# Optimization experiments

Hardware: AMD Instinct MI355X
Metric: run time of the kernel (lower is better)

The kernel has to match this reference:

```python
import jax, jax.numpy as jnp
import numpy as np

N, E, F, DH, R = 50000, 800000, 128, 128, 6  # nodes, edges, in-feat, hidden, relations (heads=1)
EPS = 1e-5
NEG_SLOPE = 0.01


def setup_inputs() -> dict:
    key = jax.random.key(0)
    ks = jax.random.split(key, 20)
    sF = 1.0 / np.sqrt(F)
    sD = 1.0 / np.sqrt(DH)
    return {
        "x": jax.random.normal(ks[0], (N, F), dtype=jnp.float32),
        "edge_index": jax.random.randint(ks[1], (2, E), 0, N, dtype=jnp.int64),
        "edge_type": jax.random.randint(ks[2], (E,), 0, R, dtype=jnp.int64),
        # RGCNConv params
        "rgcn_w": jax.random.normal(ks[3], (R, F, DH), dtype=jnp.float32) * sF,
        "rgcn_root": jax.random.normal(ks[4], (F, DH), dtype=jnp.float32) * sF,
        "rgcn_bias": jnp.zeros((DH,), dtype=jnp.float32),
        # TransformerConv params (heads=1, concat=True)
        "wq": jax.random.normal(ks[5], (DH, DH), dtype=jnp.float32) * sD,
        "bq": jnp.zeros((DH,), dtype=jnp.float32),
        "wk": jax.random.normal(ks[6], (DH, DH), dtype=jnp.float32) * sD,
        "bk": jnp.zeros((DH,), dtype=jnp.float32),
        "wv": jax.random.normal(ks[7], (DH, DH), dtype=jnp.float32) * sD,
        "bv": jnp.zeros((DH,), dtype=jnp.float32),
        "wskip": jax.random.normal(ks[8], (DH, DH), dtype=jnp.float32) * sD,
        "bskip": jnp.zeros((DH,), dtype=jnp.float32),
        # BatchNorm1d params (training-mode batch stats)
        "bn_gamma": jnp.ones((DH,), dtype=jnp.float32),
        "bn_beta": jnp.zeros((DH,), dtype=jnp.float32),
    }


def _rgcn(x, src, dst, edge_type, w, root, bias):
    # PyG RGCNConv: per-relation mean aggregation of x_j @ W_r over incoming edges, + root + bias
    out = x @ root + bias  # [N, DH]
    for r in range(R):
        m = (edge_type == r)
        xw = x @ w[r]  # [N, DH]
        msg = jnp.where(m[:, None], xw[src], 0.0)  # [E, DH]
        s = jax.ops.segment_sum(msg, dst, num_segments=N)
        cnt = jax.ops.segment_sum(m.astype(x.dtype), dst, num_segments=N)
        out = out + s / jnp.maximum(cnt, 1.0)[:, None]
    return out


def _transformer_conv(x, src, dst, wq, bq, wk, bk, wv, bv, wskip, bskip):
    # PyG TransformerConv, heads=1: edge-softmax attention over incoming edges + skip projection
    q = x @ wq + bq  # [N, DH]
    k = x @ wk + bk
    v = x @ wv + bv
    score = jnp.sum(q[dst] * k[src], axis=-1) / jnp.sqrt(jnp.asarray(DH, x.dtype))  # [E]
    smax = jax.ops.segment_max(score, dst, num_segments=N)  # -inf for empty segments (unused)
    a = jnp.exp(score - smax[dst])
    denom = jax.ops.segment_sum(a, dst, num_segments=N)
    alpha = a / denom[dst]  # every edge's dst has >=1 edge, denom > 0
    agg = jax.ops.segment_sum(alpha[:, None] * v[src], dst, num_segments=N)  # [N, DH]
    return agg + (x @ wskip + bskip)


def reference(x, edge_index, edge_type, rgcn_w, rgcn_root, rgcn_bias,
              wq, bq, wk, bk, wv, bv, wskip, bskip, bn_gamma, bn_beta):
    src, dst = edge_index[0], edge_index[1]
    h = _rgcn(x, src, dst, edge_type, rgcn_w, rgcn_root, rgcn_bias)
    h = _transformer_conv(h, src, dst, wq, bq, wk, bk, wv, bv, wskip, bskip)
    # BatchNorm1d (training: batch statistics, biased variance)
    mu = jnp.mean(h, axis=0)
    var = jnp.mean(jnp.square(h - mu), axis=0)
    h = bn_gamma * (h - mu) * jax.lax.rsqrt(var + EPS) + bn_beta
    return jnp.where(h > 0, h, NEG_SLOPE * h)
```

## Files before the change

### kernel.cpp

```cpp
#include <hip/hip_runtime.h>
#include <hip/hip_bf16.h>
#include <math.h>

#define FDIM 128
#define NREL 6

typedef _Float16 half8 __attribute__((ext_vector_type(8)));
typedef _Float16 h16x2 __attribute__((ext_vector_type(2)));
typedef float f32x4 __attribute__((ext_vector_type(4)));

#if __has_builtin(__builtin_amdgcn_fdot2)
#define FDOT2(A, B, C) __builtin_amdgcn_fdot2((A), (B), (C), false)
#else
#define FDOT2(A, B, C) ((float)(A)[0] * (float)(B)[0] + ((float)(A)[1] * (float)(B)[1] + (C)))
#endif

static __device__ __forceinline__ unsigned short f2h(float f) {
  union { _Float16 h; unsigned short u; } p; p.h = (_Float16)f; return p.u;
}

__global__ void cvt_x_kernel(const float* __restrict__ x, unsigned short* __restrict__ xh,
                             int n4) {
  int i = blockIdx.x * 256 + threadIdx.x;
  if (i < n4) {
    float4 v = ((const float4*)x)[i];
    union { _Float16 h[4]; uint2 u; } p;
    p.h[0] = (_Float16)v.x; p.h[1] = (_Float16)v.y;
    p.h[2] = (_Float16)v.z; p.h[3] = (_Float16)v.w;
    ((uint2*)xh)[i] = p.u;
  }
}

__global__ void cvt_wr_kernel(const float* __restrict__ root, const float* __restrict__ w,
                              unsigned short* __restrict__ bt) {
  int i = blockIdx.x * 256 + threadIdx.x;
  if (i < 896 * 128) {
    int n = i / 896, kk = i - n * 896;
    float v = (kk < 128) ? root[kk * 128 + n] : w[(long long)(kk - 128) * 128 + n];
    bt[i] = f2h(v);
  }
}

struct WPtrs { const float* W[4]; };
__global__ void cvt_wq_kernel(WPtrs wp, unsigned short* __restrict__ bt) {
  int i = blockIdx.x * 256 + threadIdx.x;
  if (i < 4 * 128 * 128) {
    int z = i >> 14;
    int r = i & 16383;
    int n = r >> 7, kk = r & 127;
    bt[i] = f2h(wp.W[z][kk * 128 + n]);
  }
}

struct GArgs {
  const unsigned short* Ax;
  const unsigned short* Aagg;
  const unsigned short* BtR;
  const unsigned short* BtQ;
  const float* biasR;
  const float* bias2[4];
  unsigned short* qh; unsigned short* kh; unsigned short* vh; float* sk;
  int M;
};

__launch_bounds__(256)
__global__ void gemm_fused(GArgs g) {
  __shared__ unsigned short Ah[64 * 64];
  __shared__ unsigned short Bh[128 * 64];
  __shared__ unsigned short hL[64 * 128];
  const int tid = threadIdx.x;
  const int lane = tid & 63;
  const int wid = tid >> 6;
  const int wm = wid >> 1, wn = wid & 1;
  const int lr = lane & 15, lk = lane >> 4;
  const int m0 = blockIdx.x * 64;
  const int M = g.M;

  f32x4 acc[2][4];
#pragma unroll
  for (int a = 0; a < 2; ++a)
#pragma unroll
    for (int b = 0; b < 4; ++b) { acc[a][b][0] = 0.f; acc[a][b][1] = 0.f; acc[a][b][2] = 0.f; acc[a][b][3] = 0.f; }

  for (int k0 = 0; k0 < 896; k0 += 64) {
    __syncthreads();
#pragma unroll
    for (int p = 0; p < 2; ++p) {
      int idx = tid + 256 * p;
      int r = idx >> 3, c = idx & 7;
      int row = m0 + r; if (row > M - 1) row = M - 1;
      const unsigned short* srcp =
          (k0 < 128) ? (g.Ax + (long long)row * 128 + k0 + c * 8)
                     : (g.Aagg + (long long)row * 768 + (k0 - 128) + c * 8);
      uint4 u = *(const uint4*)srcp;
      ((uint4*)Ah)[r * 8 + (c ^ (r & 7))] = u;
    }
#pragma unroll
    for (int p = 0; p < 4; ++p) {
      int idx = tid + 256 * p;
      int rn = idx >> 3, c = idx & 7;
      uint4 u = *(const uint4*)(g.BtR + (long long)rn * 896 + k0 + c * 8);
      ((uint4*)Bh)[rn * 8 + (c ^ (rn & 7))] = u;
    }
    __syncthreads();
#pragma unroll
    for (int ks = 0; ks < 2; ++ks) {
      half8 a[2], b[4];
#pragma unroll
      for (int fm = 0; fm < 2; ++fm) {
        int row = wm * 32 + fm * 16 + lr;
        a[fm] = *(const half8*)&((uint4*)Ah)[row * 8 + ((ks * 4 + lk) ^ (row & 7))];
      }
#pragma unroll
      for (int fn = 0; fn < 4; ++fn) {
        int col = wn * 64 + fn * 16 + lr;
        b[fn] = *(const half8*)&((uint4*)Bh)[col * 8 + ((ks * 4 + lk) ^ (col & 7))];
      }
#pragma unroll
      for (int fm = 0; fm < 2; ++fm)
#pragma unroll
        for (int fn = 0; fn < 4; ++fn)
          acc[fm][fn] = __builtin_amdgcn_mfma_f32_16x16x32_f16(a[fm], b[fn], acc[fm][fn], 0, 0, 0);
    }
  }

#pragma unroll
  for (int fm = 0; fm < 2; ++fm) {
#pragma unroll
    for (int fn = 0; fn < 4; ++fn) {
      int col = wn * 64 + fn * 16 + lr;
      float bv = g.biasR[col];
      int cu = col >> 3, cb = col & 7;
#pragma unroll
      for (int j = 0; j < 4; ++j) {
        int row = wm * 32 + fm * 16 + lk * 4 + j;
        float vv = acc[fm][fn][j] + bv;
        hL[row * 128 + ((cu ^ (row & 7)) << 3) + cb] = f2h(vv);
      }
    }
  }

  const float CF = 0.08838834764831845f * 1.4426950408889634f;
  const float* b2 = (wid == 0) ? g.bias2[0]
                  : (wid == 1) ? g.bias2[1]
                  : (wid == 2) ? g.bias2[2] : g.bias2[3];
#pragma unroll
  for (int half = 0; half < 2; ++half) {
    f32x4 acc2[4][4];
#pragma unroll
    for (int a = 0; a < 4; ++a)
#pragma unroll
      for (int b = 0; b < 4; ++b) { acc2[a][b][0] = 0.f; acc2[a][b][1] = 0.f; acc2[a][b][2] = 0.f; acc2[a][b][3] = 0.f; }

#pragma unroll
    for (int ks = 0; ks < 4; ++ks) {
      __syncthreads();
#pragma unroll
      for (int p = 0; p < 4; ++p) {
        int u = tid + 256 * p;
        int zz = u >> 8, n = (u >> 2) & 63, c = u & 3;
        uint4 w = *(const uint4*)(g.BtQ + (long long)zz * 16384 +
                                  (long long)(half * 64 + n) * 128 + ks * 32 + c * 8);
        ((uint4*)Bh)[zz * 256 + n * 4 + (c ^ (n & 3))] = w;
      }
      __syncthreads();
      half8 a[4], b[4];
#pragma unroll
      for (int fm = 0; fm < 4; ++fm) {
        int row = fm * 16 + lr;
        a[fm] = *(const half8*)&((uint4*)hL)[row * 16 + ((ks * 4 + lk) ^ (row & 7))];
      }
#pragma unroll
      for (int fn = 0; fn < 4; ++fn) {
        int n = fn * 16 + lr;
        b[fn] = *(const half8*)&((uint4*)Bh)[wid * 256 + n * 4 + (lk ^ (n & 3))];
      }
#pragma unroll
      for (int fm = 0; fm < 4; ++fm)
#pragma unroll
        for (int fn = 0; fn < 4; ++fn)
          acc2[fm][fn] = __builtin_amdgcn_mfma_f32_16x16x32_f16(a[fm], b[fn], acc2[fm][fn], 0, 0, 0);
    }

#pragma unroll
    for (int fm = 0; fm < 4; ++fm) {
#pragma unroll
      for (int fn = 0; fn < 4; ++fn) {
        int col = half * 64 + fn * 16 + lr;
        float bv = b2[col];
#pragma unroll
        for (int j = 0; j < 4; ++j) {
          int row = m0 + fm * 16 + lk * 4 + j;
          if (row < M) {
            float vv = acc2[fm][fn][j] + bv;
            long long off = (long long)row * 128 + col;
            if (wid == 0) g.qh[off] = f2h(vv * CF);
            else if (wid == 1) g.kh[off] = f2h(vv);
            else if (wid == 2) g.vh[off] = f2h(vv);
            else g.sk[off] = vv;
          }
        }
      }
    }
  }
}

__global__ void hist_kernel(const int* __restrict__ dst, const int* __restrict__ etype,
                            int* __restrict__ cnt, int E) {
  int e = blockIdx.x * blockDim.x + threadIdx.x;
  if (e < E) atomicAdd(&cnt[dst[e] * NREL + etype[e]], 1);
}

__launch_bounds__(1024)
__global__ void scan1(const int* __restrict__ deg, int* __restrict__ incl,
                      int* __restrict__ part, int n) {
  __shared__ int sh[1024];
  int tid = threadIdx.x;
  int i = blockIdx.x * 1024 + tid;
  sh[tid] = (i < n) ? deg[i] : 0;
  __syncthreads();
  for (int o = 1; o < 1024; o <<= 1) {
    int t = (tid >= o) ? sh[tid - o] : 0;
    __syncthreads();
    sh[tid] += t;
    __syncthreads();
  }
  if (i < n) incl[i] = sh[tid];
  if (tid == 1023) part[blockIdx.x] = sh[1023];
}

__global__ void scan2(int* part, int nb) {
  int lane = threadIdx.x;
  int run = 0;
  for (int b0 = 0; b0 < nb; b0 += 64) {
    int i = b0 + lane;
    int orig = (i < nb) ? part[i] : 0;
    int v = orig;
#pragma unroll
    for (int o = 1; o < 64; o <<= 1) {
      int t = __shfl_up(v, o);
      if (lane >= o) v += t;
    }
    if (i < nb) part[i] = run + v - orig;
    run += __shfl(v, 63);
  }
}

__global__ void scan3(const int* __restrict__ incl, const int* __restrict__ part,
                      int* __restrict__ offs, int n) {
  int i = blockIdx.x * blockDim.x + threadIdx.x;
  if (i < n) {
    offs[i + 1] = incl[i] + part[i >> 10];
    if (i == 0) offs[0] = 0;
  }
}

__global__ void scatter_kernel(const int* __restrict__ src, const int* __restrict__ dst,
                               const int* __restrict__ etype, const int* __restrict__ offs6,
                               int* __restrict__ cur, int* __restrict__ csrc, int E) {
  int e = blockIdx.x * blockDim.x + threadIdx.x;
  if (e < E) {
    int key = dst[e] * NREL + etype[e];
    int p = offs6[key] + atomicAdd(&cur[key], 1);
    csrc[p] = src[e] << 8;
  }
}

__launch_bounds__(256)
__global__ void rgcn_agg(const unsigned short* __restrict__ xh, const int* __restrict__ offs6,
                         const int* __restrict__ csrc,
                         unsigned short* __restrict__ aggh, int N) {
  int node = blockIdx.x * 4 + (threadIdx.x >> 6);
  if (node >= N) return;
  int lane = threadIdx.x & 63;
  const char* xc = (const char*)xh;
  const int* bp = offs6 + node * NREL;
  const int b0 = bp[0];
  int bn0 = bp[1], bn1 = bp[2], bn2 = bp[3], bn3 = bp[4], bn4 = bp[5], bn5 = bp[6];
  const int b6 = bn5;
  unsigned* ap = (unsigned*)(aggh + (long long)node * (NREL * FDIM)) + lane;

  float tx = 0.f, ty = 0.f;
  float px = 0.f, py = 0.f;
  int bprev = b0, snaps = 0;

#define FLUSH(EPOS)                                                          \
  while (snaps < NREL && bn0 == (EPOS)) {                                    \
    int cnt_ = (EPOS) - bprev;                                               \
    float inv_ = cnt_ ? 1.f / (float)cnt_ : 0.f;                             \
    union { _Float16 h[2]; unsigned u; } pk_;                                \
    pk_.h[0] = (_Float16)((tx - px) * inv_);                                 \
    pk_.h[1] = (_Float16)((ty - py) * inv_);                                 \
    *ap = pk_.u; ap += 64;                                                   \
    px = tx; py = ty; bprev = (EPOS); ++snaps;                               \
    bn0 = bn1; bn1 = bn2; bn2 = bn3; bn3 = bn4; bn4 = bn5;                   \
  }

#define EAT(XU)                                                              \
  {                                                                          \
    union { unsigned u; _Float16 h[2]; } c_; c_.u = (XU);                    \
    tx += (float)c_.h[0]; ty += (float)c_.h[1];                              \
  }

  FLUSH(b0)
  int e = b0;
  for (; e + 16 <= b6; e += 16) {
    unsigned xv[16];
#pragma unroll
    for (int t = 0; t < 16; ++t)
      xv[t] = ((const unsigned*)(xc + csrc[e + t]))[lane];
    EAT(xv[0])  FLUSH(e + 1)   EAT(xv[1])  FLUSH(e + 2)
    EAT(xv[2])  FLUSH(e + 3)   EAT(xv[3])  FLUSH(e + 4)
    EAT(xv[4])  FLUSH(e + 5)   EAT(xv[5])  FLUSH(e + 6)
    EAT(xv[6])  FLUSH(e + 7)   EAT(xv[7])  FLUSH(e + 8)
    EAT(xv[8])  FLUSH(e + 9)   EAT(xv[9])  FLUSH(e + 10)
    EAT(xv[10]) FLUSH(e + 11)  EAT(xv[11]) FLUSH(e + 12)
    EAT(xv[12]) FLUSH(e + 13)  EAT(xv[13]) FLUSH(e + 14)
    EAT(xv[14]) FLUSH(e + 15)  EAT(xv[15]) FLUSH(e + 16)
  }
  for (; e + 4 <= b6; e += 4) {
    unsigned y0 = ((const unsigned*)(xc + csrc[e + 0]))[lane];
    unsigned y1 = ((const unsigned*)(xc + csrc[e + 1]))[lane];
    unsigned y2 = ((const unsigned*)(xc + csrc[e + 2]))[lane];
    unsigned y3 = ((const unsigned*)(xc + csrc[e + 3]))[lane];
    EAT(y0) FLUSH(e + 1) EAT(y1) FLUSH(e + 2)
    EAT(y2) FLUSH(e + 3) EAT(y3) FLUSH(e + 4)
  }
  for (; e < b6; ++e) {
    unsigned xv = ((const unsigned*)(xc + csrc[e]))[lane];
    EAT(xv) FLUSH(e + 1)
  }
#undef EAT
#undef FLUSH
}

__launch_bounds__(256)
__global__ void attn_kernel(const unsigned short* __restrict__ qh,
                            const unsigned short* __restrict__ kh,
                            const unsigned short* __restrict__ vh,
                            const int* __restrict__ offs6, const int* __restrict__ csrc,
                            float* __restrict__ out,
                            float* __restrict__ gsumB, float* __restrict__ gsqB, int N) {
  __shared__ float bsum[4][FDIM];
  __shared__ float bsq[4][FDIM];
  int wv = threadIdx.x >> 6;
  int node = blockIdx.x * 4 + wv;
  int lane = threadIdx.x & 63;
  bool active = (node < N);
  int start = 0, end = 0;
  if (active) { start = offs6[node * NREL]; end = offs6[node * NREL + NREL]; }
  int deg = end - start;

  const int g16 = lane >> 4;
  const int f = lane & 15;
  const char* kc = (const char*)kh;
  const char* vc = (const char*)vh;

  union U4 { uint4 u; h16x2 h[4]; };
  U4 qf;
  if (active) qf.u = *(const uint4*)(qh + (long long)node * FDIM + f * 8);

  float m = -INFINITY, den = 0.f, acc0 = 0.f, acc1 = 0.f;

#define LOADQ(E0, S0, S1, S2, S3, KU, V0, V1, V2, V3)                        \
  {                                                                          \
    S0 = csrc[(E0) + (g16 ^ 0)];                                             \
    S1 = csrc[(E0) + (g16 ^ 1)];                                             \
    S2 = csrc[(E0) + (g16 ^ 2)];                                             \
    S3 = csrc[(E0) + (g16 ^ 3)];                                             \
    KU = *(const uint4*)(kc + S0 + f * 16);                                  \
    V0 = ((const unsigned*)(vc + S0))[lane];                                 \
    V1 = ((const unsigned*)(vc + S1))[lane];                                 \
    V2 = ((const unsigned*)(vc + S2))[lane];                                 \
    V3 = ((const unsigned*)(vc + S3))[lane];                                 \
  }

#define PROCESS(KU, V0, V1, V2, V3, MASKED, M0, M1, M2, M3)                  \
  {                                                                          \
    U4 kf; kf.u = KU;                                                        \
    float pd = FDOT2(qf.h[0], kf.h[0], 0.f);                                 \
    pd = FDOT2(qf.h[1], kf.h[1], pd);                                        \
    pd = FDOT2(qf.h[2], kf.h[2], pd);                                        \
    pd = FDOT2(qf.h[3], kf.h[3], pd);                                        \
    pd += __shfl_xor(pd, 1);  pd += __shfl_xor(pd, 2);                       \
    pd += __shfl_xor(pd, 4);  pd += __shfl_xor(pd, 8);                       \
    float sc0 = pd;                                                          \
    float sc1 = __shfl_xor(pd, 16);                                          \
    float sc2 = __shfl_xor(pd, 32);                                          \
    float sc3 = __shfl_xor(pd, 48);                                          \
    if (MASKED) {                                                            \
      if (!(M0)) sc0 = -INFINITY;                                            \
      if (!(M1)) sc1 = -INFINITY;                                            \
      if (!(M2)) sc2 = -INFINITY;                                            \
      if (!(M3)) sc3 = -INFINITY;                                            \
    }                                                                        \
    float mx = fmaxf(fmaxf(sc0, sc1), fmaxf(sc2, sc3));                      \
    float mn = fmaxf(m, mx);                                                 \
    float scl = exp2f(m - mn);                                               \
    float a0 = exp2f(sc0 - mn), a1 = exp2f(sc1 - mn);                        \
    float a2 = exp2f(sc2 - mn), a3 = exp2f(sc3 - mn);                        \
    den = den * scl + ((a0 + a1) + (a2 + a3));                               \
    union { unsigned u; _Float16 h[2]; } w0, w1, w2, w3;                     \
    w0.u = V0; w1.u = V1; w2.u = V2; w3.u = V3;                              \
    acc0 = acc0 * scl + a0 * (float)w0.h[0] + a1 * (float)w1.h[0]            \
                      + a2 * (float)w2.h[0] + a3 * (float)w3.h[0];           \
    acc1 = acc1 * scl + a0 * (float)w0.h[1] + a1 * (float)w1.h[1]            \
                      + a2 * (float)w2.h[1] + a3 * (float)w3.h[1];           \
    m = mn;                                                                  \
  }

  if (deg > 0) {
    int nfull4 = deg & ~3;
    int e = start;
    if (nfull4 > 0) {
      int sA0, sA1, sA2, sA3; uint4 kA; unsigned vA0, vA1, vA2, vA3;
      LOADQ(e, sA0, sA1, sA2, sA3, kA, vA0, vA1, vA2, vA3)
      for (; e < start + nfull4; e += 4) {
        int sB0, sB1, sB2, sB3; uint4 kB; unsigned vB0, vB1, vB2, vB3;
        bool more = (e + 4 < start + nfull4);
        if (more) LOADQ(e + 4, sB0, sB1, sB2, sB3, kB, vB0, vB1, vB2, vB3)
        PROCESS(kA, vA0, vA1, vA2, vA3, false, 1, 1, 1, 1)
        if (more) { kA = kB; vA0 = vB0; vA1 = vB1; vA2 = vB2; vA3 = vB3; }
      }
    }
    int rem = deg & 3;
    if (rem) {
      int e0 = start + nfull4;
      int j0 = g16 ^ 0, j1 = g16 ^ 1, j2 = g16 ^ 2, j3 = g16 ^ 3;
      int sT0 = csrc[e0 + (j0 < rem ? j0 : 0)];
      int sT1 = csrc[e0 + (j1 < rem ? j1 : 0)];
      int sT2 = csrc[e0 + (j2 < rem ? j2 : 0)];
      int sT3 = csrc[e0 + (j3 < rem ? j3 : 0)];
      uint4 kT = *(const uint4*)(kc + sT0 + f * 16);
      unsigned vT0 = ((const unsigned*)(vc + sT0))[lane];
      unsigned vT1 = ((const unsigned*)(vc + sT1))[lane];
      unsigned vT2 = ((const unsigned*)(vc + sT2))[lane];
      unsigned vT3 = ((const unsigned*)(vc + sT3))[lane];
      PROCESS(kT, vT0, vT1, vT2, vT3, true, j0 < rem, j1 < rem, j2 < rem, j3 < rem)
    }
  }
#undef LOADQ
#undef PROCESS

  float2 o = make_float2(0.f, 0.f);
  if (active) {
    float2* op = (float2*)(out + (long long)node * FDIM);
    o = op[lane];
    if (deg > 0) {
      float inv = 1.f / den;
      o.x += acc0 * inv;
      o.y += acc1 * inv;
      op[lane] = o;
    }
  }

  ((float2*)bsum[wv])[lane] = make_float2(o.x, o.y);
  ((float2*)bsq[wv])[lane]  = make_float2(o.x * o.x, o.y * o.y);
  __syncthreads();
  if (threadIdx.x < FDIM) {
    int d = threadIdx.x;
    float s  = bsum[0][d] + bsum[1][d] + bsum[2][d] + bsum[3][d];
    float q2 = bsq[0][d]  + bsq[1][d]  + bsq[2][d]  + bsq[3][d];
    int bucket = blockIdx.x & 31;
    atomicAdd(&gsumB[bucket * FDIM + d], s);
    atomicAdd(&gsqB[bucket * FDIM + d], q2);
  }
}

__global__ void bn_final(const float* __restrict__ gsumB, const float* __restrict__ gsqB,
                         const float* __restrict__ gamma, const float* __restrict__ beta,
                         float* __restrict__ ss, int N) {
  int d = threadIdx.x;
  if (d < FDIM) {
    float s = 0.f, q = 0.f;
    for (int b = 0; b < 32; ++b) { s += gsumB[b * FDIM + d]; q += gsqB[b * FDIM + d]; }
    float mean = s / (float)N;
    float var = q / (float)N - mean * mean;
    var = fmaxf(var, 0.f);
    float sc = gamma[d] * rsqrtf(var + 1e-5f);
    ss[d] = sc;
    ss[FDIM + d] = beta[d] - mean * sc;
  }
}

__global__ void bn_apply(float* __restrict__ x, const float* __restrict__ ss, long long total4) {
  long long i = (long long)blockIdx.x * blockDim.x + threadIdx.x;
  if (i < total4) {
    int d0 = (int)((i * 4) & (FDIM - 1));
    float4 vv = ((const float4*)x)[i];
    float y0 = ss[d0 + 0] * vv.x + ss[FDIM + d0 + 0];
    float y1 = ss[d0 + 1] * vv.y + ss[FDIM + d0 + 1];
    float y2 = ss[d0 + 2] * vv.z + ss[FDIM + d0 + 2];
    float y3 = ss[d0 + 3] * vv.w + ss[FDIM + d0 + 3];
    vv.x = (y0 > 0.f) ? y0 : 0.01f * y0;
    vv.y = (y1 > 0.f) ? y1 : 0.01f * y1;
    vv.z = (y2 > 0.f) ? y2 : 0.01f * y2;
    vv.w = (y3 > 0.f) ? y3 : 0.01f * y3;
    ((float4*)x)[i] = vv;
  }
}

extern "C" void kernel_launch(void* const* d_in, const int* in_sizes, int n_in,
                              void* d_out, int out_size, void* d_ws, size_t ws_size,
                              hipStream_t stream) {
  const float* x         = (const float*)d_in[0];
  const int*   ei        = (const int*)d_in[1];
  const int*   etype     = (const int*)d_in[2];
  const float* rgcn_w    = (const float*)d_in[3];
  const float* rgcn_root = (const float*)d_in[4];
  const float* rgcn_bias = (const float*)d_in[5];
  const float* wq = (const float*)d_in[6];  const float* bq = (const float*)d_in[7];
  const float* wk = (const float*)d_in[8];  const float* bk = (const float*)d_in[9];
  const float* wv = (const float*)d_in[10]; const float* bv = (const float*)d_in[11];
  const float* wsk = (const float*)d_in[12]; const float* bsk = (const float*)d_in[13];
  const float* gamma = (const float*)d_in[14]; const float* beta = (const float*)d_in[15];

  const int N = in_sizes[0] / FDIM;
  const int E = in_sizes[1] / 2;
  const int* src = ei;
  const int* dst = ei + E;
  const int NK = N * NREL;

  char* base = (char*)d_ws;
  size_t off = 0;
  auto alloc = [&](size_t bytes) -> char* {
    char* p = base + off;
    off += (bytes + 255) & ~(size_t)255;
    return p;
  };
  unsigned short* aggh = (unsigned short*)alloc((size_t)N * (NREL * FDIM) * 2);
  unsigned short* qbuf = aggh;
  unsigned short* kbuf = aggh + (size_t)N * FDIM;
  unsigned short* vbuf = aggh + 2 * (size_t)N * FDIM;
  unsigned short* xh   = (unsigned short*)alloc((size_t)N * FDIM * 2);
  unsigned short* btR  = (unsigned short*)alloc((size_t)896 * 128 * 2);
  unsigned short* btQ  = (unsigned short*)alloc((size_t)4 * 128 * 128 * 2);
  int* cnt6 = (int*)alloc((size_t)2 * NK * 4);
  int* cur  = cnt6 + NK;
  int* offs6 = (int*)alloc((size_t)(NK + 1) * 4);
  int* incl = (int*)alloc((size_t)NK * 4);
  int* part = (int*)alloc((size_t)512 * 4);
  int* csrc = (int*)alloc((size_t)E * 4);
  float* gsumB = (float*)alloc((size_t)32 * FDIM * 4);
  float* gsqB  = (float*)alloc((size_t)32 * FDIM * 4);
  float* ss    = (float*)alloc((size_t)2 * FDIM * 4);

  float* out = (float*)d_out;

  hipMemsetAsync(cnt6, 0, (size_t)2 * NK * sizeof(int), stream);
  hipMemsetAsync(gsumB, 0, (size_t)64 * FDIM * sizeof(float), stream);

  int n4 = N * FDIM / 4;
  cvt_x_kernel<<<(n4 + 255) / 256, 256, 0, stream>>>(x, xh, n4);
  cvt_wr_kernel<<<(896 * 128 + 255) / 256, 256, 0, stream>>>(rgcn_root, rgcn_w, btR);
  WPtrs wp; wp.W[0] = wq; wp.W[1] = wk; wp.W[2] = wv; wp.W[3] = wsk;
  cvt_wq_kernel<<<(4 * 128 * 128 + 255) / 256, 256, 0, stream>>>(wp, btQ);

  hist_kernel<<<(E + 255) / 256, 256, 0, stream>>>(dst, etype, cnt6, E);
  int nb = (NK + 1023) / 1024;
  scan1<<<nb, 1024, 0, stream>>>(cnt6, incl, part, NK);
  scan2<<<1, 64, 0, stream>>>(part, nb);
  scan3<<<(NK + 255) / 256, 256, 0, stream>>>(incl, part, offs6, NK);
  scatter_kernel<<<(E + 255) / 256, 256, 0, stream>>>(src, dst, etype, offs6, cur, csrc, E);

  const int nodeBlocks = (N + 3) / 4;
  const int gemmBlocks = (N + 63) / 64;

  rgcn_agg<<<nodeBlocks, 256, 0, stream>>>(xh, offs6, csrc, aggh, N);

  GArgs g = {};
  g.Ax = xh; g.Aagg = aggh; g.BtR = btR; g.BtQ = btQ;
  g.biasR = rgcn_bias;
  g.bias2[0] = bq; g.bias2[1] = bk; g.bias2[2] = bv; g.bias2[3] = bsk;
  g.qh = qbuf; g.kh = kbuf; g.vh = vbuf; g.sk = out;
  g.M = N;
  gemm_fused<<<gemmBlocks, 256, 0, stream>>>(g);

  attn_kernel<<<nodeBlocks, 256, 0, stream>>>(qbuf, kbuf, vbuf, offs6, csrc, out,
                                              gsumB, gsqB, N);

  bn_final<<<1, 128, 0, stream>>>(gsumB, gsqB, gamma, beta, ss, N);
  long long total4 = (long long)N * FDIM / 4;
  bn_apply<<<(int)((total4 + 255) / 256), 256, 0, stream>>>(out, ss, total4);
}
```

Measured before the change: 331.6 us.

## Read GEMM B operands directly from global memory and double-buffer A tiles

```diff
diff --git a/kernel.cpp b/kernel.cpp
--- a/kernel.cpp
+++ b/kernel.cpp
@@ -65,8 +65,7 @@
 
 __launch_bounds__(256)
 __global__ void gemm_fused(GArgs g) {
-  __shared__ unsigned short Ah[64 * 64];
-  __shared__ unsigned short Bh[128 * 64];
+  __shared__ unsigned short Ah[2][64 * 64];
   __shared__ unsigned short hL[64 * 128];
   const int tid = threadIdx.x;
   const int lane = tid & 63;
@@ -76,45 +75,46 @@
   const int m0 = blockIdx.x * 64;
   const int M = g.M;
 
+#define STAGE_A(BUF, K0)                                                     \
+  {                                                                          \
+    _Pragma("unroll")                                                        \
+    for (int p = 0; p < 2; ++p) {                                            \
+      int idx = tid + 256 * p;                                               \
+      int r = idx >> 3, c = idx & 7;                                         \
+      int row = m0 + r; if (row > M - 1) row = M - 1;                        \
+      const unsigned short* srcp =                                           \
+          ((K0) < 128) ? (g.Ax + (long long)row * 128 + (K0) + c * 8)        \
+                       : (g.Aagg + (long long)row * 768 + ((K0) - 128) + c * 8); \
+      uint4 u = *(const uint4*)srcp;                                         \
+      ((uint4*)Ah[BUF])[r * 8 + (c ^ (r & 7))] = u;                          \
+    }                                                                        \
+  }
+
   f32x4 acc[2][4];
 #pragma unroll
   for (int a = 0; a < 2; ++a)
 #pragma unroll
     for (int b = 0; b < 4; ++b) { acc[a][b][0] = 0.f; acc[a][b][1] = 0.f; acc[a][b][2] = 0.f; acc[a][b][3] = 0.f; }
 
-  for (int k0 = 0; k0 < 896; k0 += 64) {
+  STAGE_A(0, 0)
+  int cur = 0;
+#pragma unroll 1
+  for (int it = 0; it < 14; ++it) {
     __syncthreads();
-#pragma unroll
-    for (int p = 0; p < 2; ++p) {
-      int idx = tid + 256 * p;
-      int r = idx >> 3, c = idx & 7;
-      int row = m0 + r; if (row > M - 1) row = M - 1;
-      const unsigned short* srcp =
-          (k0 < 128) ? (g.Ax + (long long)row * 128 + k0 + c * 8)
-                     : (g.Aagg + (long long)row * 768 + (k0 - 128) + c * 8);
-      uint4 u = *(const uint4*)srcp;
-      ((uint4*)Ah)[r * 8 + (c ^ (r & 7))] = u;
-    }
-#pragma unroll
-    for (int p = 0; p < 4; ++p) {
-      int idx = tid + 256 * p;
-      int rn = idx >> 3, c = idx & 7;
-      uint4 u = *(const uint4*)(g.BtR + (long long)rn * 896 + k0 + c * 8);
-      ((uint4*)Bh)[rn * 8 + (c ^ (rn & 7))] = u;
-    }
-    __syncthreads();
+    if (it + 1 < 14) STAGE_A(cur ^ 1, (it + 1) * 64)
+    const int k0 = it * 64;
 #pragma unroll
     for (int ks = 0; ks < 2; ++ks) {
       half8 a[2], b[4];
 #pragma unroll
       for (int fm = 0; fm < 2; ++fm) {
         int row = wm * 32 + fm * 16 + lr;
-        a[fm] = *(const half8*)&((uint4*)Ah)[row * 8 + ((ks * 4 + lk) ^ (row & 7))];
+        a[fm] = *(const half8*)&((uint4*)Ah[cur])[row * 8 + ((ks * 4 + lk) ^ (row & 7))];
       }
 #pragma unroll
       for (int fn = 0; fn < 4; ++fn) {
         int col = wn * 64 + fn * 16 + lr;
-        b[fn] = *(const half8*)&((uint4*)Bh)[col * 8 + ((ks * 4 + lk) ^ (col & 7))];
+        b[fn] = *(const half8*)(g.BtR + (long long)col * 896 + k0 + ks * 32 + lk * 8);
       }
 #pragma unroll
       for (int fm = 0; fm < 2; ++fm)
@@ -122,7 +122,9 @@
         for (int fn = 0; fn < 4; ++fn)
           acc[fm][fn] = __builtin_amdgcn_mfma_f32_16x16x32_f16(a[fm], b[fn], acc[fm][fn], 0, 0, 0);
     }
-  }
+    cur ^= 1;
+  }
+#undef STAGE_A
 
 #pragma unroll
   for (int fm = 0; fm < 2; ++fm) {
@@ -139,11 +141,13 @@
       }
     }
   }
+  __syncthreads();
 
   const float CF = 0.08838834764831845f * 1.4426950408889634f;
   const float* b2 = (wid == 0) ? g.bias2[0]
                   : (wid == 1) ? g.bias2[1]
                   : (wid == 2) ? g.bias2[2] : g.bias2[3];
+  const unsigned short* Wz = g.BtQ + (long long)wid * 16384;
 #pragma unroll
   for (int half = 0; half < 2; ++half) {
     f32x4 acc2[4][4];
@@ -154,16 +158,6 @@
 
 #pragma unroll
     for (int ks = 0; ks < 4; ++ks) {
-      __syncthreads();
-#pragma unroll
-      for (int p = 0; p < 4; ++p) {
-        int u = tid + 256 * p;
-        int zz = u >> 8, n = (u >> 2) & 63, c = u & 3;
-        uint4 w = *(const uint4*)(g.BtQ + (long long)zz * 16384 +
-                                  (long long)(half * 64 + n) * 128 + ks * 32 + c * 8);
-        ((uint4*)Bh)[zz * 256 + n * 4 + (c ^ (n & 3))] = w;
-      }
-      __syncthreads();
       half8 a[4], b[4];
 #pragma unroll
       for (int fm = 0; fm < 4; ++fm) {
@@ -172,8 +166,8 @@
       }
 #pragma unroll
       for (int fn = 0; fn < 4; ++fn) {
-        int n = fn * 16 + lr;
-        b[fn] = *(const half8*)&((uint4*)Bh)[wid * 256 + n * 4 + (lk ^ (n & 3))];
+        int n = half * 64 + fn * 16 + lr;
+        b[fn] = *(const half8*)(Wz + (long long)n * 128 + ks * 32 + lk * 8);
       }
 #pragma unroll
       for (int fm = 0; fm < 4; ++fm)
```

New measurement: 368.1 us (median of 2 runs). 11.0% more time.
